# Kernel tuning notes

Measured on AMD Instinct MI355X. Metric: run time of the kernel, lower is better.

The kernel has to match this reference:

```python
import jax, jax.numpy as jnp
import numpy as np

N, E, LE, C = 20000, 320000, 640000, 128
EPS = 1e-7  # GENConv message eps


def _ln(x, g, b):
    # torch.nn.LayerNorm, eps=1e-5
    m = jnp.mean(x, axis=-1, keepdims=True)
    v = jnp.var(x, axis=-1, keepdims=True)
    return (x - m) * jax.lax.rsqrt(v + 1e-5) * g + b


def _mlp(x, W1, b1, g, b, W2, b2):
    # GENConv MLP, num_layers=2, norm='layer': Linear -> LayerNorm -> ReLU -> Linear
    h = jax.nn.relu(_ln(x @ W1 + b1, g, b))
    return h @ W2 + b2


def _gen_deep(x, src, dst, edge_attr, num_nodes, p):
    # DeepGCNLayer 'res+': norm -> relu -> dropout(eval=identity) -> GENConv -> + x
    h = jax.nn.relu(_ln(x, p['pre_g'], p['pre_b']))
    # GENConv message: relu(x_j [+ edge_attr]) + eps
    msg = h[src]
    if edge_attr is not None:
        msg = msg + edge_attr
    msg = jax.nn.relu(msg) + EPS  # [E, C]
    # softmax aggregation per destination segment, per channel
    logits = msg * p['t']
    mx = jax.ops.segment_max(logits, dst, num_segments=num_nodes)
    alpha = jnp.exp(logits - mx[dst])
    denom = jax.ops.segment_sum(alpha, dst, num_segments=num_nodes)
    aggr = jax.ops.segment_sum(alpha * msg, dst, num_segments=num_nodes)
    aggr = aggr / jnp.where(denom == 0, 1.0, denom)
    out = aggr + h  # GENConv root skip: out + x_r
    out = _mlp(out, p['W1'], p['b1'], p['ln_g'], p['ln_b'], p['W2'], p['b2'])
    return x + out  # res+ residual


def setup_inputs() -> dict:
    key = jax.random.key(0)
    ks = iter(jax.random.split(key, 16))
    s = 0.05
    d = {}
    d['v_x'] = jax.random.normal(next(ks), (N, C), jnp.float32)
    d['e_x'] = jax.random.normal(next(ks), (E, C), jnp.float32)
    d['v_edge_index'] = jax.random.randint(next(ks), (2, E), 0, N)
    d['e_edge_index'] = jax.random.randint(next(ks), (2, LE), 0, E)
    for pfx in ('e_', 'n_'):
        d[pfx + 'pre_g'] = jnp.ones((C,), jnp.float32)
        d[pfx + 'pre_b'] = jnp.zeros((C,), jnp.float32)
        d[pfx + 't'] = jnp.array(1.0, jnp.float32)
        d[pfx + 'W1'] = jax.random.normal(next(ks), (C, 2 * C), jnp.float32) * s
        d[pfx + 'b1'] = jnp.zeros((2 * C,), jnp.float32)
        d[pfx + 'ln_g'] = jnp.ones((2 * C,), jnp.float32)
        d[pfx + 'ln_b'] = jnp.zeros((2 * C,), jnp.float32)
        d[pfx + 'W2'] = jax.random.normal(next(ks), (2 * C, C), jnp.float32) * s
        d[pfx + 'b2'] = jnp.zeros((C,), jnp.float32)
    return d


def reference(v_x, e_x, v_edge_index, e_edge_index,
              e_pre_g, e_pre_b, e_t, e_W1, e_b1, e_ln_g, e_ln_b, e_W2, e_b2,
              n_pre_g, n_pre_b, n_t, n_W1, n_b1, n_ln_g, n_ln_b, n_W2, n_b2):
    ep = dict(pre_g=e_pre_g, pre_b=e_pre_b, t=e_t, W1=e_W1, b1=e_b1,
              ln_g=e_ln_g, ln_b=e_ln_b, W2=e_W2, b2=e_b2)
    npar = dict(pre_g=n_pre_g, pre_b=n_pre_b, t=n_t, W1=n_W1, b1=n_b1,
                ln_g=n_ln_g, ln_b=n_ln_b, W2=n_W2, b2=n_b2)
    # edge layer: GENConv over the line graph (no edge_attr)
    e_out = _gen_deep(e_x, e_edge_index[0], e_edge_index[1], None, E, ep)
    # node layer: GENConv over node graph with updated edge features as edge_attr
    v_out = _gen_deep(v_x, v_edge_index[0], v_edge_index[1], e_out, N, npar)
    return (v_out, e_out)
```

## Files before the change

kernel.cpp:

```cpp
#include <hip/hip_runtime.h>
#include <hip/hip_bf16.h>

#define GEN_EPS 1e-7f

typedef __attribute__((ext_vector_type(8))) short short8;
typedef __attribute__((ext_vector_type(4))) float f32x4;

__global__ void count_all(const int* __restrict__ e_dst, const int* __restrict__ v_dst,
                          int* __restrict__ ce, int* __restrict__ cn,
                          unsigned long long* __restrict__ part, int LE, int En) {
  if (blockIdx.x == 0) {
    for (int k = threadIdx.x; k < 1024; k += 256) part[k] = 0ULL;
  }
  int i = blockIdx.x * 256 + threadIdx.x;
  if (i < LE)
    atomicAdd(&ce[e_dst[i]], 1);
  else if (i < LE + En)
    atomicAdd(&cn[v_dst[i - LE]], 1);
}

__global__ void prep_all(
    const float* __restrict__ eW1, const float* __restrict__ eW2,
    const float* __restrict__ nW1, const float* __restrict__ nW2,
    short* __restrict__ eW1P, short* __restrict__ eW2P, short* __restrict__ nW1P,
    short* __restrict__ nW2P,
    const float* __restrict__ ex, const float* __restrict__ vx,
    const float* __restrict__ eg, const float* __restrict__ eb,
    const float* __restrict__ ng, const float* __restrict__ nb_,
    __hip_bfloat16* __restrict__ he, __hip_bfloat16* __restrict__ hn, int E, int N) {
  int b = blockIdx.x;
  int tid = threadIdx.x;

  if (b < 768) {
    const float* W;
    short* WP;
    int R, Cc, c;
    if (b < 256) {
      W = eW1; WP = eW1P; R = 128; Cc = 256; c = b;
    } else if (b < 384) {
      W = eW2; WP = eW2P; R = 256; Cc = 128; c = b - 256;
    } else if (b < 640) {
      W = nW1; WP = nW1P; R = 128; Cc = 256; c = b - 384;
    } else {
      W = nW2; WP = nW2P; R = 256; Cc = 128; c = b - 640;
    }
    size_t tbase = (size_t)(c >> 4) * (size_t)(16 * R);
    int rsub = c & 15;
    for (int k = tid; k < R; k += blockDim.x) {
      __hip_bfloat16 bv = __float2bfloat16(W[(size_t)k * Cc + c]);
      int kk = k & 31;
      WP[tbase + (size_t)(k >> 5) * 512 + (kk >> 3) * 128 + rsub * 8 + (kk & 7)] =
          *(short*)&bv;
    }
    return;
  }
  b -= 768;

  int l32 = tid & 31;
  int rr = b * 8 + ((tid & 255) >> 5);
  const float* x;
  const float* g;
  const float* bb;
  __hip_bfloat16* h;
  int r;
  if (rr < E) {
    x = ex; g = eg; bb = eb; h = he; r = rr;
  } else if (rr < E + N) {
    x = vx; g = ng; bb = nb_; h = hn; r = rr - E;
  } else {
    return;
  }
  float4 v = ((const float4*)(x + (size_t)r * 128))[l32];
  float s = v.x + v.y + v.z + v.w;
#pragma unroll
  for (int o = 16; o; o >>= 1) s += __shfl_xor(s, o);
  float m = s * (1.0f / 128.0f);
  float d0 = v.x - m, d1 = v.y - m, d2 = v.z - m, d3 = v.w - m;
  float q = d0 * d0 + d1 * d1 + d2 * d2 + d3 * d3;
#pragma unroll
  for (int o = 16; o; o >>= 1) q += __shfl_xor(q, o);
  float rstd = rsqrtf(q * (1.0f / 128.0f) + 1e-5f);
  float4 gv = ((const float4*)g)[l32];
  float4 bv = ((const float4*)bb)[l32];
  float2 h01, h23;
  h01.x = fmaxf(fmaf(d0 * rstd, gv.x, bv.x), 0.0f);
  h01.y = fmaxf(fmaf(d1 * rstd, gv.y, bv.y), 0.0f);
  h23.x = fmaxf(fmaf(d2 * rstd, gv.z, bv.z), 0.0f);
  h23.y = fmaxf(fmaf(d3 * rstd, gv.w, bv.w), 0.0f);
  __hip_bfloat162 p0 = __float22bfloat162_rn(h01);
  __hip_bfloat162 p1 = __float22bfloat162_rn(h23);
  uint2 u;
  u.x = *(uint*)&p0;
  u.y = *(uint*)&p1;
  ((uint2*)(h + (size_t)r * 128))[l32] = u;
}

__global__ void scan_fused(const int* __restrict__ ce, const int* __restrict__ cn,
                           unsigned long long* __restrict__ part,
                           int* __restrict__ off_e, int* __restrict__ off_n,
                           int* __restrict__ cur_e, int* __restrict__ cur_n,
                           int nbE, int E, int N, int LE, int En) {
  __shared__ int sm[256];
  __shared__ int smPrev;
  int b = blockIdx.x;
  const int* counts;
  int M, nnz, bb;
  int* off;
  int* cursor;
  unsigned long long* pr;
  if (b < nbE) {
    counts = ce; M = E; nnz = LE; bb = b; off = off_e; cursor = cur_e; pr = part;
  } else {
    counts = cn; M = N; nnz = En; bb = b - nbE; off = off_n; cursor = cur_n;
    pr = part + 512;
  }
  int t = threadIdx.x;
  int base = bb * 1024 + t * 4;
  int c[4];
  int s = 0;
#pragma unroll
  for (int i = 0; i < 4; i++) {
    int idx = base + i;
    c[i] = (idx < M) ? counts[idx] : 0;
    s += c[i];
  }
  sm[t] = s;
  __syncthreads();
  for (int o = 1; o < 256; o <<= 1) {
    int v = (t >= o) ? sm[t - o] : 0;
    __syncthreads();
    sm[t] += v;
    __syncthreads();
  }
  int total = sm[255];
  if (t == 0) {
    int prev = 0;
    if (bb == 0) {
      atomicExch(&pr[0], (2ULL << 32) | (unsigned long long)(unsigned)total);
    } else {
      atomicExch(&pr[bb], (1ULL << 32) | (unsigned long long)(unsigned)total);
      int j = bb - 1;
      while (true) {
        unsigned long long v;
        do {
          v = atomicAdd(&pr[j], 0ULL);
        } while ((v >> 32) == 0ULL);
        prev += (int)(v & 0xffffffffULL);
        if ((v >> 32) == 2ULL) break;
        j--;
      }
      atomicExch(&pr[bb], (2ULL << 32) | (unsigned long long)(unsigned)(prev + total));
    }
    smPrev = prev;
  }
  __syncthreads();
  int p = smPrev + sm[t] - s;
#pragma unroll
  for (int i = 0; i < 4; i++) {
    int idx = base + i;
    if (idx < M) {
      off[idx] = p;
      cursor[idx] = p;
      p += c[i];
    }
  }
  if (bb == 0 && t == 0) off[M] = nnz;
}

__global__ void fill_all(const int* __restrict__ e_src, const int* __restrict__ e_dst,
                         const int* __restrict__ v_src, const int* __restrict__ v_dst,
                         int* __restrict__ cur_e, int* __restrict__ cur_n,
                         int* __restrict__ csrs_e, int* __restrict__ csrs_n,
                         int* __restrict__ csre_n, int LE, int En) {
  int i = blockIdx.x * blockDim.x + threadIdx.x;
  if (i < LE) {
    int p = atomicAdd(&cur_e[e_dst[i]], 1);
    csrs_e[p] = e_src[i];
  } else if (i < LE + En) {
    int j = i - LE;
    int p = atomicAdd(&cur_n[v_dst[j]], 1);
    csrs_n[p] = v_src[j];
    csre_n[p] = j;
  }
}

template <bool HAS_EATTR>
__global__ __launch_bounds__(256) void aggregate_kernel(
    const __hip_bfloat16* __restrict__ h, const int* __restrict__ off,
    const int* __restrict__ csr_src, const int* __restrict__ csr_eid,
    const ushort* __restrict__ eattr, const float* __restrict__ tptr,
    uint* __restrict__ yP, int M) {
  int lane = threadIdx.x & 63;
  int r = blockIdx.x * 4 + (threadIdx.x >> 6);
  if (r >= M) return;
  const float t = tptr[0];
  float2 hv = __bfloat1622float2(((const __hip_bfloat162*)(h + (size_t)r * 128))[lane]);
  int e0 = off[r], e1 = off[r + 1];
  float d0 = 0.0f, d1 = 0.0f, a0 = 0.0f, a1 = 0.0f;
  for (int e = e0; e < e1; e += 4) {
    int n = e1 - e;
    float2 mv[4];
#pragma unroll
    for (int u = 0; u < 4; u++) {
      int ee = (u < n) ? e + u : e;
      int s = csr_src[ee];
      mv[u] = __bfloat1622float2(((const __hip_bfloat162*)(h + (size_t)s * 128))[lane]);
    }
    if (HAS_EATTR) {
#pragma unroll
      for (int u = 0; u < 4; u++) {
        int ee = (u < n) ? e + u : e;
        int id = csr_eid[ee];
        uint ea = ((const uint*)(eattr + (size_t)id * 128))[lane];
        float2 ef = __bfloat1622float2(*(__hip_bfloat162*)&ea);
        mv[u].x += ef.x;
        mv[u].y += ef.y;
      }
    }
#pragma unroll
    for (int u = 0; u < 4; u++) {
      float w = (u < n) ? 1.0f : 0.0f;
      float m0 = fmaxf(mv[u].x, 0.0f) + GEN_EPS;
      float m1 = fmaxf(mv[u].y, 0.0f) + GEN_EPS;
      float al0 = __expf(m0 * t) * w, al1 = __expf(m1 * t) * w;
      d0 += al0;
      d1 += al1;
      a0 = fmaf(al0, m0, a0);
      a1 = fmaf(al1, m1, a1);
    }
  }
  float2 yv;
  yv.x = (e1 > e0 ? a0 / d0 : 0.0f) + hv.x;
  yv.y = (e1 > e0 ? a1 / d1 : 0.0f) + hv.y;
  __hip_bfloat162 yb2 = __float22bfloat162_rn(yv);
  yP[(r >> 4) * 1024 + (lane >> 4) * 256 + (r & 15) * 16 + (lane & 15)] = *(uint*)&yb2;
}

template <bool WRITE_BF16>
__global__ __launch_bounds__(512, 2) void mlp_kernel(
    const float* __restrict__ x, const short* yP, const short* __restrict__ W1P,
    const float* __restrict__ b1, const float* __restrict__ lng,
    const float* __restrict__ lnb, const short* __restrict__ W2P,
    const float* __restrict__ b2, float* __restrict__ out, ushort* out16,
    int ntiles, int stride, int M) {
  __shared__ short W1s[128 * 256];
  __shared__ short W2s[256 * 128];
  __shared__ short scr[8][2][16 * 34];

  const int tid = threadIdx.x, lane = tid & 63, wv = tid >> 6;
  const int rA = lane & 15, hi = lane >> 4;
  const int kA = hi * 8, jrow = hi * 4;
  const int foW = lane * 8;
  const int foA = rA * 32 + kA;

  {
    const short8* g1 = (const short8*)W1P;
    short8* l1 = (short8*)W1s;
#pragma unroll
    for (int i = 0; i < 8; i++) l1[i * 512 + tid] = g1[i * 512 + tid];
    const short8* g2 = (const short8*)W2P;
    short8* l2 = (short8*)W2s;
#pragma unroll
    for (int i = 0; i < 8; i++) l2[i * 512 + tid] = g2[i * 512 + tid];
  }

  float b1v[16], lngv[16], lnbv[16], b2v[8];
#pragma unroll
  for (int ct = 0; ct < 16; ct++) {
    int col = ct * 16 + rA;
    b1v[ct] = b1[col];
    lngv[ct] = lng[col];
    lnbv[ct] = lnb[col];
  }
#pragma unroll
  for (int ct = 0; ct < 8; ct++) b2v[ct] = b2[ct * 16 + rA];

  __syncthreads();

  int t = blockIdx.x * 8 + wv;
  short8 yA0, yA1, yA2, yA3;
  if (t < ntiles) {
    const short* yb = yP + (size_t)t * 2048 + foA;
    yA0 = *(const short8*)(yb);
    yA1 = *(const short8*)(yb + 512);
    yA2 = *(const short8*)(yb + 1024);
    yA3 = *(const short8*)(yb + 1536);
  }

  for (; t < ntiles; t += stride) {
    const int row0 = t * 16;

    f32x4 C1[16];
#pragma unroll
    for (int i = 0; i < 16; i++) C1[i] = (f32x4)0.0f;
#pragma unroll
    for (int kc = 0; kc < 4; kc++) {
      short8 a = (kc == 0) ? yA0 : (kc == 1) ? yA1 : (kc == 2) ? yA2 : yA3;
#pragma unroll
      for (int ct = 0; ct < 16; ct++) {
        short8 B = *(const short8*)&W1s[(ct * 4 + kc) * 512 + foW];
        C1[ct] = __builtin_amdgcn_mfma_f32_16x16x32_bf16(a, B, C1[ct], 0, 0, 0);
      }
    }

    {
      int tn = t + stride;
      int tc = (tn < ntiles) ? tn : t;
      const short* yb = yP + (size_t)tc * 2048 + foA;
      yA0 = *(const short8*)(yb);
      yA1 = *(const short8*)(yb + 512);
      yA2 = *(const short8*)(yb + 1024);
      yA3 = *(const short8*)(yb + 1536);
    }

    float xv[32];
#pragma unroll
    for (int ct = 0; ct < 8; ct++)
#pragma unroll
      for (int j = 0; j < 4; j++) {
        int row = row0 + jrow + j;
        int rr = (row < M) ? row : (M - 1);
        xv[ct * 4 + j] = x[(size_t)rr * 128 + ct * 16 + rA];
      }

#pragma unroll
    for (int ct = 0; ct < 16; ct++)
#pragma unroll
      for (int j = 0; j < 4; j++) C1[ct][j] += b1v[ct];

    float mean[4], rstd[4];
#pragma unroll
    for (int j = 0; j < 4; j++) {
      float p = 0.0f, q = 0.0f;
#pragma unroll
      for (int ct = 0; ct < 16; ct++) {
        p += C1[ct][j];
        q = fmaf(C1[ct][j], C1[ct][j], q);
      }
#pragma unroll
      for (int o = 1; o < 16; o <<= 1) {
        p += __shfl_xor(p, o);
        q += __shfl_xor(q, o);
      }
      float m = p * (1.0f / 256.0f);
      mean[j] = m;
      rstd[j] = rsqrtf(q * (1.0f / 256.0f) - m * m + 1e-5f);
    }

    f32x4 C2[8];
#pragma unroll
    for (int i = 0; i < 8; i++) C2[i] = (f32x4)0.0f;
#pragma unroll
    for (int kc = 0; kc < 8; kc++) {
      short* s = &scr[wv][kc & 1][0];
#pragma unroll
      for (int ct2 = 0; ct2 < 2; ct2++) {
        int ctg = kc * 2 + ct2;
#pragma unroll
        for (int j = 0; j < 4; j++) {
          float v =
              fmaxf(fmaf((C1[ctg][j] - mean[j]) * rstd[j], lngv[ctg], lnbv[ctg]), 0.0f);
          __hip_bfloat16 bv = __float2bfloat16(v);
          s[(jrow + j) * 34 + ct2 * 16 + rA] = *(short*)&bv;
        }
      }
      asm volatile("s_waitcnt lgkmcnt(0)" ::: "memory");
      __builtin_amdgcn_sched_barrier(0);
      short8 a = *(const short8*)&s[rA * 34 + kA];
#pragma unroll
      for (int ct = 0; ct < 8; ct++) {
        short8 B = *(const short8*)&W2s[(ct * 8 + kc) * 512 + foW];
        C2[ct] = __builtin_amdgcn_mfma_f32_16x16x32_bf16(a, B, C2[ct], 0, 0, 0);
      }
    }

#pragma unroll
    for (int ct = 0; ct < 8; ct++) {
#pragma unroll
      for (int j = 0; j < 4; j++) {
        int row = row0 + jrow + j;
        if (row < M) {
          size_t idx = (size_t)row * 128 + ct * 16 + rA;
          float o = C2[ct][j] + b2v[ct] + xv[ct * 4 + j];
          out[idx] = o;
          if (WRITE_BF16) {
            __hip_bfloat16 bo = __float2bfloat16(o);
            out16[idx] = *(ushort*)&bo;
          }
        }
      }
    }
  }
}

extern "C" void kernel_launch(void* const* d_in, const int* in_sizes, int n_in,
                              void* d_out, int out_size, void* d_ws, size_t ws_size,
                              hipStream_t stream) {
  const int C = 128;
  const float* v_x = (const float*)d_in[0];
  const float* e_x = (const float*)d_in[1];
  const int* v_ei = (const int*)d_in[2];
  const int* e_ei = (const int*)d_in[3];
  const int N = in_sizes[0] / C;
  const int E = in_sizes[1] / C;
  const int LE = in_sizes[3] / 2;

  const float* ep[9];
  const float* np_[9];
  for (int i = 0; i < 9; i++) ep[i] = (const float*)d_in[4 + i];
  for (int i = 0; i < 9; i++) np_[i] = (const float*)d_in[13 + i];

  float* v_out = (float*)d_out;
  float* e_out = (float*)d_out + (size_t)N * C;

  char* wsp = (char*)d_ws;
  size_t o = 0;
  auto carve = [&](size_t bytes) {
    void* p = wsp + o;
    o += (bytes + 255) & ~(size_t)255;
    return p;
  };
  short* yPe = (short*)carve((size_t)E * C * 2);
  short* yPn = (short*)carve((size_t)N * C * 2);
  int* counts = (int*)carve((size_t)(E + N) * 4);
  int* off_e = (int*)carve(((size_t)E + 1) * 4);
  int* off_n = (int*)carve(((size_t)N + 1) * 4);
  int* cur_e = (int*)carve((size_t)E * 4);
  int* cur_n = (int*)carve((size_t)N * 4);
  unsigned long long* part = (unsigned long long*)carve(1024 * 8);
  int* csrs_e = (int*)carve((size_t)LE * 4);
  int* csrs_n = (int*)carve((size_t)E * 4);
  int* csre_n = (int*)carve((size_t)E * 4);
  short* eW1P = (short*)carve((size_t)256 * 128 * 2);
  short* eW2P = (short*)carve((size_t)128 * 256 * 2);
  short* nW1P = (short*)carve((size_t)256 * 128 * 2);
  short* nW2P = (short*)carve((size_t)128 * 256 * 2);
  (void)ws_size;
  (void)n_in;
  (void)out_size;

  int* counts_e = counts;
  int* counts_n = counts + E;
  __hip_bfloat16* h_e = (__hip_bfloat16*)e_out;
  __hip_bfloat16* h_n = (__hip_bfloat16*)v_out;

  hipMemsetAsync(counts, 0, (size_t)(E + N) * 4, stream);
  count_all<<<(LE + E + 255) / 256, 256, 0, stream>>>(e_ei + LE, v_ei + E, counts_e,
                                                      counts_n, part, LE, E);
  int nLN = (E + N + 7) / 8;
  prep_all<<<768 + nLN, 256, 0, stream>>>(ep[3], ep[7], np_[3], np_[7], eW1P, eW2P,
                                          nW1P, nW2P, e_x, v_x, ep[0], ep[1], np_[0],
                                          np_[1], h_e, h_n, E, N);
  int nbE = (E + 1023) / 1024, nbN = (N + 1023) / 1024;
  scan_fused<<<nbE + nbN, 256, 0, stream>>>(counts_e, counts_n, part, off_e, off_n,
                                            cur_e, cur_n, nbE, E, N, LE, E);
  fill_all<<<(LE + E + 255) / 256, 256, 0, stream>>>(e_ei, e_ei + LE, v_ei, v_ei + E,
                                                     cur_e, cur_n, csrs_e, csrs_n, csre_n,
                                                     LE, E);

  aggregate_kernel<false><<<(E + 3) / 4, 256, 0, stream>>>(h_e, off_e, csrs_e, nullptr,
                                                           nullptr, ep[2], (uint*)yPe, E);
  {
    int ntiles = (E + 15) / 16;
    int gblocks = (ntiles + 7) / 8;
    if (gblocks > 256) gblocks = 256;
    int stride = gblocks * 8;
    mlp_kernel<true><<<gblocks, 512, 0, stream>>>(e_x, yPe, eW1P, ep[4], ep[5], ep[6],
                                                  eW2P, ep[8], e_out, (ushort*)yPe,
                                                  ntiles, stride, E);
  }

  aggregate_kernel<true><<<(N + 3) / 4, 256, 0, stream>>>(h_n, off_n, csrs_n, csre_n,
                                                          (const ushort*)yPe, np_[2],
                                                          (uint*)yPn, N);
  {
    int ntiles = (N + 15) / 16;
    int gblocks = (ntiles + 7) / 8;
    if (gblocks > 256) gblocks = 256;
    int stride = gblocks * 8;
    mlp_kernel<false><<<gblocks, 512, 0, stream>>>(v_x, yPn, nW1P, np_[4], np_[5], np_[6],
                                                   nW2P, np_[8], v_out, nullptr, ntiles,
                                                   stride, N);
  }
}
```

Before: 410.9 us.

## Fuse degree counting into prep kernel and prefetch residual rows in MLP

Removes the separate count_all launch by giving prep_all extra blocks that do the destination-degree atomics, and zeroes the scan partials buffer with a single memset by placing it right after counts. In the MLP kernel, the residual x rows for the next tile are loaded alongside the next A fragments, before the current tile's epilogue. This cuts one launch and hides global load latency, but adds 32 live registers per thread, which may lower occupancy.

```diff
diff --git a/kernel.cpp b/kernel.cpp
--- a/kernel.cpp
+++ b/kernel.cpp
@@ -5,25 +5,14 @@
 
 typedef __attribute__((ext_vector_type(8))) short short8;
 typedef __attribute__((ext_vector_type(4))) float f32x4;
-
-__global__ void count_all(const int* __restrict__ e_dst, const int* __restrict__ v_dst,
-                          int* __restrict__ ce, int* __restrict__ cn,
-                          unsigned long long* __restrict__ part, int LE, int En) {
-  if (blockIdx.x == 0) {
-    for (int k = threadIdx.x; k < 1024; k += 256) part[k] = 0ULL;
-  }
-  int i = blockIdx.x * 256 + threadIdx.x;
-  if (i < LE)
-    atomicAdd(&ce[e_dst[i]], 1);
-  else if (i < LE + En)
-    atomicAdd(&cn[v_dst[i - LE]], 1);
-}
 
 __global__ void prep_all(
     const float* __restrict__ eW1, const float* __restrict__ eW2,
     const float* __restrict__ nW1, const float* __restrict__ nW2,
     short* __restrict__ eW1P, short* __restrict__ eW2P, short* __restrict__ nW1P,
     short* __restrict__ nW2P,
+    const int* __restrict__ e_dst, const int* __restrict__ v_dst,
+    int* __restrict__ ce, int* __restrict__ cn, int LE, int En, int nCNT,
     const float* __restrict__ ex, const float* __restrict__ vx,
     const float* __restrict__ eg, const float* __restrict__ eb,
     const float* __restrict__ ng, const float* __restrict__ nb_,
@@ -55,6 +44,16 @@
     return;
   }
   b -= 768;
+
+  if (b < nCNT) {
+    int i = b * 256 + tid;
+    if (i < LE)
+      atomicAdd(&ce[e_dst[i]], 1);
+    else if (i < LE + En)
+      atomicAdd(&cn[v_dst[i - LE]], 1);
+    return;
+  }
+  b -= nCNT;
 
   int l32 = tid & 31;
   int rr = b * 8 + ((tid & 255) >> 5);
@@ -279,12 +278,21 @@
 
   int t = blockIdx.x * 8 + wv;
   short8 yA0, yA1, yA2, yA3;
+  float xv[32];
   if (t < ntiles) {
     const short* yb = yP + (size_t)t * 2048 + foA;
     yA0 = *(const short8*)(yb);
     yA1 = *(const short8*)(yb + 512);
     yA2 = *(const short8*)(yb + 1024);
     yA3 = *(const short8*)(yb + 1536);
+#pragma unroll
+    for (int ct = 0; ct < 8; ct++)
+#pragma unroll
+      for (int j = 0; j < 4; j++) {
+        int row = t * 16 + jrow + j;
+        int rr = (row < M) ? row : (M - 1);
+        xv[ct * 4 + j] = x[(size_t)rr * 128 + ct * 16 + rA];
+      }
   }
 
   for (; t < ntiles; t += stride) {
@@ -303,6 +311,7 @@
       }
     }
 
+    float xvN[32];
     {
       int tn = t + stride;
       int tc = (tn < ntiles) ? tn : t;
@@ -311,17 +320,15 @@
       yA1 = *(const short8*)(yb + 512);
       yA2 = *(const short8*)(yb + 1024);
       yA3 = *(const short8*)(yb + 1536);
-    }
-
-    float xv[32];
-#pragma unroll
-    for (int ct = 0; ct < 8; ct++)
-#pragma unroll
-      for (int j = 0; j < 4; j++) {
-        int row = row0 + jrow + j;
-        int rr = (row < M) ? row : (M - 1);
-        xv[ct * 4 + j] = x[(size_t)rr * 128 + ct * 16 + rA];
-      }
+#pragma unroll
+      for (int ct = 0; ct < 8; ct++)
+#pragma unroll
+        for (int j = 0; j < 4; j++) {
+          int row = tc * 16 + jrow + j;
+          int rr = (row < M) ? row : (M - 1);
+          xvN[ct * 4 + j] = x[(size_t)rr * 128 + ct * 16 + rA];
+        }
+    }
 
 #pragma unroll
     for (int ct = 0; ct < 16; ct++)
@@ -390,6 +397,8 @@
         }
       }
     }
+#pragma unroll
+    for (int i = 0; i < 32; i++) xv[i] = xvN[i];
   }
 }
 
@@ -423,11 +432,11 @@
   short* yPe = (short*)carve((size_t)E * C * 2);
   short* yPn = (short*)carve((size_t)N * C * 2);
   int* counts = (int*)carve((size_t)(E + N) * 4);
+  unsigned long long* part = (unsigned long long*)carve(1024 * 8);
   int* off_e = (int*)carve(((size_t)E + 1) * 4);
   int* off_n = (int*)carve(((size_t)N + 1) * 4);
   int* cur_e = (int*)carve((size_t)E * 4);
   int* cur_n = (int*)carve((size_t)N * 4);
-  unsigned long long* part = (unsigned long long*)carve(1024 * 8);
   int* csrs_e = (int*)carve((size_t)LE * 4);
   int* csrs_n = (int*)carve((size_t)E * 4);
   int* csre_n = (int*)carve((size_t)E * 4);
@@ -444,13 +453,14 @@
   __hip_bfloat16* h_e = (__hip_bfloat16*)e_out;
   __hip_bfloat16* h_n = (__hip_bfloat16*)v_out;
 
-  hipMemsetAsync(counts, 0, (size_t)(E + N) * 4, stream);
-  count_all<<<(LE + E + 255) / 256, 256, 0, stream>>>(e_ei + LE, v_ei + E, counts_e,
-                                                      counts_n, part, LE, E);
+  size_t counts_pad = (((size_t)(E + N) * 4) + 255) & ~(size_t)255;
+  hipMemsetAsync(counts, 0, counts_pad + 1024 * 8, stream);
+  int nCNT = (LE + E + 255) / 256;
   int nLN = (E + N + 7) / 8;
-  prep_all<<<768 + nLN, 256, 0, stream>>>(ep[3], ep[7], np_[3], np_[7], eW1P, eW2P,
-                                          nW1P, nW2P, e_x, v_x, ep[0], ep[1], np_[0],
-                                          np_[1], h_e, h_n, E, N);
+  prep_all<<<768 + nCNT + nLN, 256, 0, stream>>>(
+      ep[3], ep[7], np_[3], np_[7], eW1P, eW2P, nW1P, nW2P, e_ei + LE, v_ei + E,
+      counts_e, counts_n, LE, E, nCNT, e_x, v_x, ep[0], ep[1], np_[0], np_[1], h_e, h_n,
+      E, N);
   int nbE = (E + 1023) / 1024, nbN = (N + 1023) / 1024;
   scan_fused<<<nbE + nbN, 256, 0, stream>>>(counts_e, counts_n, part, off_e, off_n,
                                             cur_e, cur_n, nbE, E, N, LE, E);
```

Result: no change. 415.3 us (+1.1%).
